# Kernel tuning notes

Measured on AMD Instinct MI355X. Metric: run time of the kernel, lower is better.

Reference implementation:

```python
import jax, jax.numpy as jnp
import numpy as np

N, E, F, HID, HEADS, L, OUT = 100000, 1600000, 16, 64, 2, 3, 200
EPS = 1e-5

def leaky(x, s):
    return jnp.where(x >= 0, x, s * x)

def layer_norm(x, g, b):
    m = jnp.mean(x, axis=-1, keepdims=True)
    v = jnp.mean(jnp.square(x - m), axis=-1, keepdims=True)
    return (x - m) * jax.lax.rsqrt(v + EPS) * g + b

def gat_conv(h, src, dst, W, a_src, a_dst, bias, n_nodes):
    # h: [N, HID]; W: [HID, HEADS*HID]; a_src/a_dst: [HEADS, HID]; bias: [HID]
    hp = (h @ W).reshape(n_nodes, HEADS, HID)            # [N, H, C]
    al_src = jnp.einsum('nhc,hc->nh', hp, a_src)          # [N, H]
    al_dst = jnp.einsum('nhc,hc->nh', hp, a_dst)
    e = leaky(al_src[src] + al_dst[dst], 0.2)             # [E', H]
    emax = jax.ops.segment_max(e, dst, num_segments=n_nodes)
    ee = jnp.exp(e - emax[dst])
    denom = jax.ops.segment_sum(ee, dst, num_segments=n_nodes)
    alpha = ee / (denom[dst] + 1e-16)                     # segment softmax over incoming edges
    msg = hp[src] * alpha[:, :, None]                     # [E', H, C]
    out = jax.ops.segment_sum(msg, dst, num_segments=n_nodes)  # [N, H, C]
    return jnp.mean(out, axis=1) + bias                   # concat=False -> head mean

def setup_inputs():
    key = jax.random.key(0)
    ks = jax.random.split(key, 16)
    rn = lambda k, s, sc=0.1: jax.random.normal(k, s, jnp.float32) * sc
    return {
        'x': jax.random.normal(ks[0], (N, F), jnp.float32),
        'edge_index': jax.random.randint(ks[1], (2, E), 0, N),
        'emb_w': rn(ks[2], (F, HID)), 'emb_b': jnp.zeros((HID,), jnp.float32),
        'emb_g': jnp.ones((HID,), jnp.float32), 'emb_beta': jnp.zeros((HID,), jnp.float32),
        'lin_w': rn(ks[3], (L, HID, HEADS * HID)),
        'att_src': rn(ks[4], (L, HEADS, HID)), 'att_dst': rn(ks[5], (L, HEADS, HID)),
        'conv_b': jnp.zeros((L, HID), jnp.float32),
        'ln_g': jnp.ones((L, HID), jnp.float32), 'ln_b': jnp.zeros((L, HID), jnp.float32),
        'fc1_w': rn(ks[6], (HID, HID)), 'fc1_b': jnp.zeros((HID,), jnp.float32),
        'fcn_g': jnp.ones((HID,), jnp.float32), 'fcn_b': jnp.zeros((HID,), jnp.float32),
        'fc2_w': rn(ks[7], (HID, OUT)), 'fc2_b': jnp.zeros((OUT,), jnp.float32),
    }

def reference(x, edge_index, emb_w, emb_b, emb_g, emb_beta, lin_w, att_src, att_dst,
              conv_b, ln_g, ln_b, fc1_w, fc1_b, fcn_g, fcn_b, fc2_w, fc2_b):
    n = x.shape[0]
    loops = jnp.arange(n)
    src = jnp.concatenate([edge_index[0], loops])  # PyG GATConv adds self-loops
    dst = jnp.concatenate([edge_index[1], loops])
    h = leaky(layer_norm(x @ emb_w + emb_b, emb_g, emb_beta), 0.1)
    for i in range(lin_w.shape[0]):
        h = gat_conv(h, src, dst, lin_w[i], att_src[i], att_dst[i], conv_b[i], n)
        h = leaky(layer_norm(h, ln_g[i], ln_b[i]), 0.1)
    g = jnp.mean(h, axis=0, keepdims=True)  # no batch vector -> global mean pool
    g = leaky(layer_norm(g @ fc1_w + fc1_b, fcn_g, fcn_b), 0.1)
    return jax.nn.sigmoid(g @ fc2_w + fc2_b)
```

## Files before the change

### kernel.cpp

```cpp
#include <hip/hip_runtime.h>
#include <hip/hip_bf16.h>
#include <math.h>

typedef __attribute__((ext_vector_type(8))) short short8v;
typedef __attribute__((ext_vector_type(4))) float float4v;

__device__ __forceinline__ float wsum(float v) {
#pragma unroll
  for (int s = 32; s > 0; s >>= 1) v += __shfl_xor(v, s, 64);
  return v;
}
__device__ __forceinline__ float bcast(float v, int l) {
  return __int_as_float(__builtin_amdgcn_readlane(__float_as_int(v), l));
}
__device__ __forceinline__ int bcasti(int v, int l) {
  return __builtin_amdgcn_readlane(v, l);
}
__device__ __forceinline__ unsigned bf16bits(float f) {
  unsigned u = __float_as_uint(f);
  return (u + 0x7fffu + ((u >> 16) & 1u)) >> 16;
}

__global__ void k_embed(const float* __restrict__ x, const float* __restrict__ w,
                        const float* __restrict__ b, const float* __restrict__ g,
                        const float* __restrict__ beta, short* __restrict__ hb, int n) {
  __shared__ float ws[16 * 64];
  for (int i = threadIdx.x; i < 16 * 64; i += blockDim.x) ws[i] = w[i];
  __syncthreads();
  int wid = (blockIdx.x * blockDim.x + threadIdx.x) >> 6;
  int lane = threadIdx.x & 63;
  if (wid >= n) return;
  const float* xr = x + (size_t)wid * 16;
  float acc = b[lane];
#pragma unroll
  for (int k = 0; k < 16; ++k) acc = fmaf(xr[k], ws[k * 64 + lane], acc);
  float mean = wsum(acc) * 0.015625f;
  float xc = acc - mean;
  float var = wsum(xc * xc) * 0.015625f;
  float y = xc * rsqrtf(var + 1e-5f) * g[lane] + beta[lane];
  y = (y >= 0.f) ? y : 0.1f * y;
  hb[(size_t)wid * 64 + lane] = (short)bf16bits(y);
}

__global__ void k_deg(const int* __restrict__ ei, int E, int n, int* __restrict__ deg,
                      int* __restrict__ pos) {
  int i = blockIdx.x * blockDim.x + threadIdx.x;
  int tot = E + n;
  if (i >= tot) return;
  int d = (i < E) ? ei[E + i] : (i - E);
  pos[i] = atomicAdd(&deg[d], 1);
}

__global__ void k_scanA(const int* __restrict__ deg, int n, int* __restrict__ texcl,
                        int* __restrict__ bsum) {
  __shared__ int sh[256];
  int bid = blockIdx.x, tid = threadIdx.x;
  int base = bid * 2048 + tid * 8;
  int s = 0;
#pragma unroll
  for (int i = 0; i < 8; ++i) {
    int idx = base + i;
    s += (idx < n) ? deg[idx] : 0;
  }
  sh[tid] = s;
  __syncthreads();
  for (int st = 1; st < 256; st <<= 1) {
    int t = (tid >= st) ? sh[tid - st] : 0;
    __syncthreads();
    sh[tid] += t;
    __syncthreads();
  }
  texcl[bid * 256 + tid] = sh[tid] - s;
  if (tid == 255) bsum[bid] = sh[255];
}

__global__ void k_scanB(int* __restrict__ bsum, int nb) {
  __shared__ int sh[256];
  int tid = threadIdx.x;
  int v = (tid < nb) ? bsum[tid] : 0;
  sh[tid] = v;
  __syncthreads();
  for (int st = 1; st < 256; st <<= 1) {
    int t = (tid >= st) ? sh[tid - st] : 0;
    __syncthreads();
    sh[tid] += t;
    __syncthreads();
  }
  if (tid < nb) bsum[tid] = sh[tid] - v;
}

__global__ void k_scanC(const int* __restrict__ deg, int n, const int* __restrict__ texcl,
                        const int* __restrict__ bsum, int* __restrict__ off, int total) {
  int bid = blockIdx.x, tid = threadIdx.x;
  int run = bsum[bid] + texcl[bid * 256 + tid];
  int base = bid * 2048 + tid * 8;
#pragma unroll
  for (int i = 0; i < 8; ++i) {
    int idx = base + i;
    if (idx < n) {
      off[idx] = run;
      run += deg[idx];
    }
  }
  if (bid == 0 && tid == 0) off[n] = total;
}

__global__ void k_scatter(const int* __restrict__ ei, int E, int n,
                          const int* __restrict__ off, const int* __restrict__ pos,
                          int* __restrict__ csr) {
  int i = blockIdx.x * blockDim.x + threadIdx.x;
  int tot = E + n;
  if (i >= tot) return;
  int s, d;
  if (i < E) { s = ei[i]; d = ei[E + i]; } else { s = i - E; d = i - E; }
  csr[off[d] + pos[i]] = s;
}

__global__ __launch_bounds__(256) void k_hp(
    const short* __restrict__ hb, const float* __restrict__ W,
    const float* __restrict__ asrc, const float* __restrict__ adst,
    unsigned* __restrict__ hp2, float2* __restrict__ al_s, float2* __restrict__ al_d,
    int n) {
  __shared__ short wlds[16 * 64 * 8];
  int tid = threadIdx.x;
  for (int idx = tid; idx < 1024; idx += 256) {
    int fr = idx >> 6;
    int ls = idx & 63;
    int kb = (fr >> 3) * 32 + (ls >> 4) * 8;
    int c = (fr & 7) * 16 + (ls & 15);
    short tmp[8];
#pragma unroll
    for (int j = 0; j < 8; ++j)
      tmp[j] = (short)bf16bits(W[(size_t)(kb + j) * 128 + c]);
    *reinterpret_cast<short8v*>(&wlds[idx * 8]) = *reinterpret_cast<const short8v*>(tmp);
  }
  __syncthreads();
  int lane = tid & 63;
  int nb = (blockIdx.x * 4 + (tid >> 6)) * 16;
  if (nb >= n) return;
  int col = lane & 15, kg = lane >> 4;
  int rowA = nb + col;
  if (rowA > n - 1) rowA = n - 1;
  const short8v* aptr = reinterpret_cast<const short8v*>(hb + (size_t)rowA * 64 + kg * 8);
  short8v af0 = aptr[0];
  short8v af1 = aptr[4];
  float ps0[4] = {0, 0, 0, 0}, ps1[4] = {0, 0, 0, 0};
  float pd0[4] = {0, 0, 0, 0}, pd1[4] = {0, 0, 0, 0};
#pragma unroll
  for (int ctp = 0; ctp < 4; ++ctp) {
    const short8v* bp0 = reinterpret_cast<const short8v*>(&wlds[((0 * 8 + ctp) * 64 + lane) * 8]);
    const short8v* bp1 = reinterpret_cast<const short8v*>(&wlds[((1 * 8 + ctp) * 64 + lane) * 8]);
    float4v accA = {0.f, 0.f, 0.f, 0.f};
    accA = __builtin_amdgcn_mfma_f32_16x16x32_bf16(af0, *bp0, accA, 0, 0, 0);
    accA = __builtin_amdgcn_mfma_f32_16x16x32_bf16(af1, *bp1, accA, 0, 0, 0);
    const short8v* bq0 = reinterpret_cast<const short8v*>(&wlds[((0 * 8 + ctp + 4) * 64 + lane) * 8]);
    const short8v* bq1 = reinterpret_cast<const short8v*>(&wlds[((1 * 8 + ctp + 4) * 64 + lane) * 8]);
    float4v accB = {0.f, 0.f, 0.f, 0.f};
    accB = __builtin_amdgcn_mfma_f32_16x16x32_bf16(af0, *bq0, accB, 0, 0, 0);
    accB = __builtin_amdgcn_mfma_f32_16x16x32_bf16(af1, *bq1, accB, 0, 0, 0);
    int c = ctp * 16 + col;
    float a_s0 = asrc[c], a_s1 = asrc[64 + c];
    float a_d0 = adst[c], a_d1 = adst[64 + c];
#pragma unroll
    for (int r = 0; r < 4; ++r) {
      int node = nb + kg * 4 + r;
      unsigned pk = bf16bits(accA[r]) | (bf16bits(accB[r]) << 16);
      if (node < n) hp2[(size_t)node * 64 + c] = pk;
      ps0[r] = fmaf(accA[r], a_s0, ps0[r]);
      ps1[r] = fmaf(accB[r], a_s1, ps1[r]);
      pd0[r] = fmaf(accA[r], a_d0, pd0[r]);
      pd1[r] = fmaf(accB[r], a_d1, pd1[r]);
    }
  }
#pragma unroll
  for (int m = 1; m < 16; m <<= 1) {
#pragma unroll
    for (int r = 0; r < 4; ++r) {
      ps0[r] += __shfl_xor(ps0[r], m, 64);
      ps1[r] += __shfl_xor(ps1[r], m, 64);
      pd0[r] += __shfl_xor(pd0[r], m, 64);
      pd1[r] += __shfl_xor(pd1[r], m, 64);
    }
  }
  if (col == 0) {
#pragma unroll
    for (int r = 0; r < 4; ++r) {
      int node = nb + kg * 4 + r;
      if (node < n) {
        al_s[node] = make_float2(ps0[r], ps1[r]);
        al_d[node] = make_float2(pd0[r], pd1[r]);
      }
    }
  }
}

__global__ void k_gat(const unsigned* __restrict__ hp2, const float* __restrict__ al_s,
                      const float* __restrict__ al_d, const int* __restrict__ off,
                      const int* __restrict__ csr, const float* __restrict__ bias,
                      const float* __restrict__ g, const float* __restrict__ b,
                      short* __restrict__ hb, int n) {
  int gw = (blockIdx.x * blockDim.x + threadIdx.x) >> 6;
  if (gw >= n) return;
  int node = __builtin_amdgcn_readfirstlane(gw);
  int lane = threadIdx.x & 63;
  const float2* al2 = (const float2*)al_s;
  float2 adv = ((const float2*)al_d)[node];
  int beg = off[node], end = off[node + 1];
  float acc0 = 0.f, acc1 = 0.f, dnl0 = 0.f, dnl1 = 0.f;
  for (int cb = beg; cb < end; cb += 64) {
    int jj = cb + lane;
    int sv = 0;
    float w0v = 0.f, w1v = 0.f;
    if (jj < end) {
      sv = csr[jj];
      float2 e = al2[sv];
      float e0 = e.x + adv.x; e0 = (e0 >= 0.f) ? e0 : 0.2f * e0;
      float e1 = e.y + adv.y; e1 = (e1 >= 0.f) ? e1 : 0.2f * e1;
      w0v = __expf(e0);
      w1v = __expf(e1);
    }
    dnl0 += w0v; dnl1 += w1v;
    int cnt = min(64, end - cb);
    int t = 0;
    for (; t + 4 <= cnt; t += 4) {
      int sA = bcasti(sv, t), sB = bcasti(sv, t + 1);
      int sC = bcasti(sv, t + 2), sD = bcasti(sv, t + 3);
      float wA0 = bcast(w0v, t), wA1 = bcast(w1v, t);
      float wB0 = bcast(w0v, t + 1), wB1 = bcast(w1v, t + 1);
      float wC0 = bcast(w0v, t + 2), wC1 = bcast(w1v, t + 2);
      float wD0 = bcast(w0v, t + 3), wD1 = bcast(w1v, t + 3);
      unsigned uA = hp2[(size_t)sA * 64 + lane];
      unsigned uB = hp2[(size_t)sB * 64 + lane];
      unsigned uC = hp2[(size_t)sC * 64 + lane];
      unsigned uD = hp2[(size_t)sD * 64 + lane];
      acc0 = fmaf(wA0, __uint_as_float(uA << 16), acc0);
      acc1 = fmaf(wA1, __uint_as_float(uA & 0xffff0000u), acc1);
      acc0 = fmaf(wB0, __uint_as_float(uB << 16), acc0);
      acc1 = fmaf(wB1, __uint_as_float(uB & 0xffff0000u), acc1);
      acc0 = fmaf(wC0, __uint_as_float(uC << 16), acc0);
      acc1 = fmaf(wC1, __uint_as_float(uC & 0xffff0000u), acc1);
      acc0 = fmaf(wD0, __uint_as_float(uD << 16), acc0);
      acc1 = fmaf(wD1, __uint_as_float(uD & 0xffff0000u), acc1);
    }
    for (; t < cnt; ++t) {
      int s = bcasti(sv, t);
      float w0 = bcast(w0v, t), w1 = bcast(w1v, t);
      unsigned u = hp2[(size_t)s * 64 + lane];
      acc0 = fmaf(w0, __uint_as_float(u << 16), acc0);
      acc1 = fmaf(w1, __uint_as_float(u & 0xffff0000u), acc1);
    }
  }
  float dn0 = wsum(dnl0), dn1 = wsum(dnl1);
  float oc = 0.5f * (acc0 / (dn0 + 1e-16f) + acc1 / (dn1 + 1e-16f)) + bias[lane];
  float mean = wsum(oc) * 0.015625f;
  float xc = oc - mean;
  float var = wsum(xc * xc) * 0.015625f;
  float y = xc * rsqrtf(var + 1e-5f) * g[lane] + b[lane];
  y = (y >= 0.f) ? y : 0.1f * y;
  hb[(size_t)node * 64 + lane] = (short)bf16bits(y);
}

__global__ void k_pool(const short* __restrict__ hb, float* __restrict__ gsum, int n) {
  __shared__ float sh[256];
  int col = threadIdx.x & 63;
  int rw = threadIdx.x >> 6;
  float acc = 0.f;
  for (long r = (long)blockIdx.x * 4 + rw; r < n; r += (long)gridDim.x * 4) {
    unsigned u = (unsigned)(unsigned short)hb[r * 64 + col];
    acc += __uint_as_float(u << 16);
  }
  sh[threadIdx.x] = acc;
  __syncthreads();
  if (threadIdx.x < 64) {
    float s = sh[threadIdx.x] + sh[64 + threadIdx.x] + sh[128 + threadIdx.x] +
              sh[192 + threadIdx.x];
    atomicAdd(&gsum[col], s);
  }
}

__global__ void k_head(const float* __restrict__ gsum, const float* __restrict__ fc1w,
                       const float* __restrict__ fc1b, const float* __restrict__ fng,
                       const float* __restrict__ fnb, const float* __restrict__ fc2w,
                       const float* __restrict__ fc2b, float* __restrict__ out,
                       float invN) {
  __shared__ float t[64];
  __shared__ float gl[64];
  int tid = threadIdx.x;
  if (tid < 64) gl[tid] = gsum[tid] * invN;
  __syncthreads();
  if (tid < 64) {
    float z = fc1b[tid];
    for (int k = 0; k < 64; ++k) z = fmaf(gl[k], fc1w[k * 64 + tid], z);
    float mean = wsum(z) * 0.015625f;
    float xc = z - mean;
    float var = wsum(xc * xc) * 0.015625f;
    float y = xc * rsqrtf(var + 1e-5f) * fng[tid] + fnb[tid];
    t[tid] = (y >= 0.f) ? y : 0.1f * y;
  }
  __syncthreads();
  if (tid < 200) {
    float o = fc2b[tid];
    for (int k = 0; k < 64; ++k) o = fmaf(t[k], fc2w[k * 200 + tid], o);
    out[tid] = 1.f / (1.f + expf(-o));
  }
}

extern "C" void kernel_launch(void* const* d_in, const int* in_sizes, int n_in,
                              void* d_out, int out_size, void* d_ws, size_t ws_size,
                              hipStream_t stream) {
  const float* x      = (const float*)d_in[0];
  const int*   ei     = (const int*)d_in[1];
  const float* emb_w  = (const float*)d_in[2];
  const float* emb_b  = (const float*)d_in[3];
  const float* emb_g  = (const float*)d_in[4];
  const float* emb_be = (const float*)d_in[5];
  const float* lin_w  = (const float*)d_in[6];
  const float* att_s  = (const float*)d_in[7];
  const float* att_d  = (const float*)d_in[8];
  const float* conv_b = (const float*)d_in[9];
  const float* ln_g   = (const float*)d_in[10];
  const float* ln_b   = (const float*)d_in[11];
  const float* fc1_w  = (const float*)d_in[12];
  const float* fc1_b  = (const float*)d_in[13];
  const float* fcn_g  = (const float*)d_in[14];
  const float* fcn_b  = (const float*)d_in[15];
  const float* fc2_w  = (const float*)d_in[16];
  const float* fc2_b  = (const float*)d_in[17];
  float* out = (float*)d_out;

  int N = in_sizes[0] / 16;
  int E = in_sizes[1] / 2;
  int tot = E + N;
  int nb_scan = (N + 2047) / 2048;

  char* p = (char*)d_ws;
  auto alloc = [&](size_t bytes) {
    char* r = p;
    p += (bytes + 255) & ~(size_t)255;
    return r;
  };
  short*    hb    = (short*)alloc((size_t)N * 64 * 2);
  unsigned* hp2   = (unsigned*)alloc((size_t)N * 64 * 4);
  float2*   al_s  = (float2*)alloc((size_t)N * 8);
  float2*   al_d  = (float2*)alloc((size_t)N * 8);
  int*      deg   = (int*)alloc((size_t)N * 4);
  int*      off   = (int*)alloc((size_t)(N + 1) * 4);
  int*      pos   = (int*)alloc((size_t)tot * 4);
  int*      csr   = (int*)alloc((size_t)tot * 4);
  float*    gsum  = (float*)alloc(64 * 4);
  int*      texcl = (int*)alloc((size_t)nb_scan * 256 * 4);
  int*      bsum  = (int*)alloc((size_t)nb_scan * 4);

  hipMemsetAsync(deg, 0, (size_t)N * 4, stream);
  hipMemsetAsync(gsum, 0, 64 * 4, stream);

  int eb = (tot + 255) / 256;
  k_deg<<<eb, 256, 0, stream>>>(ei, E, N, deg, pos);
  k_scanA<<<nb_scan, 256, 0, stream>>>(deg, N, texcl, bsum);
  k_scanB<<<1, 256, 0, stream>>>(bsum, nb_scan);
  k_scanC<<<nb_scan, 256, 0, stream>>>(deg, N, texcl, bsum, off, tot);
  k_scatter<<<eb, 256, 0, stream>>>(ei, E, N, off, pos, csr);

  int nbe = (N + 3) / 4;
  k_embed<<<nbe, 256, 0, stream>>>(x, emb_w, emb_b, emb_g, emb_be, hb, N);

  int nbh = (N + 63) / 64;
  for (int l = 0; l < 3; ++l) {
    k_hp<<<nbh, 256, 0, stream>>>(hb, lin_w + (size_t)l * 64 * 128, att_s + l * 128,
                                  att_d + l * 128, hp2, al_s, al_d, N);
    k_gat<<<nbe, 256, 0, stream>>>(hp2, (const float*)al_s, (const float*)al_d, off,
                                   csr, conv_b + l * 64, ln_g + l * 64, ln_b + l * 64,
                                   hb, N);
  }

  k_pool<<<1024, 256, 0, stream>>>(hb, gsum, N);
  k_head<<<1, 256, 0, stream>>>(gsum, fc1_w, fc1_b, fcn_g, fcn_b, fc2_w, fc2_b, out,
                                1.0f / (float)N);
}
```

Measured before the change: 519.6 us.

## Stage edge records in LDS and gather two edges per wave step

Each wave now writes its chunk of edge records (source index and the two head weights) to shared memory instead of broadcasting them with readlane. Each half-wave then handles a different edge per step, with every lane loading 8 bytes (two bf16 pairs) of the source row. The two halves' partial sums are combined at the end with cross-lane shuffles. This aims to cut scalar broadcast overhead and halve the number of gather load instructions per edge. In exchange it adds LDS traffic, a small shuffle epilogue, and relies on wave-local ordering of the LDS buffer with no explicit barrier.

Measured after the change: 524.9 us. No clear change (+1.0%).

```diff
diff --git a/kernel.cpp b/kernel.cpp
--- a/kernel.cpp
+++ b/kernel.cpp
@@ -9,12 +9,6 @@
 #pragma unroll
   for (int s = 32; s > 0; s >>= 1) v += __shfl_xor(v, s, 64);
   return v;
-}
-__device__ __forceinline__ float bcast(float v, int l) {
-  return __int_as_float(__builtin_amdgcn_readlane(__float_as_int(v), l));
-}
-__device__ __forceinline__ int bcasti(int v, int l) {
-  return __builtin_amdgcn_readlane(v, l);
 }
 __device__ __forceinline__ unsigned bf16bits(float f) {
   unsigned u = __float_as_uint(f);
@@ -199,14 +193,19 @@
                       const int* __restrict__ csr, const float* __restrict__ bias,
                       const float* __restrict__ g, const float* __restrict__ b,
                       short* __restrict__ hb, int n) {
+  __shared__ uint4 recs[4][64];
   int gw = (blockIdx.x * blockDim.x + threadIdx.x) >> 6;
   if (gw >= n) return;
   int node = __builtin_amdgcn_readfirstlane(gw);
   int lane = threadIdx.x & 63;
+  int wslot = (threadIdx.x >> 6) & 3;
+  int hl = lane & 31;
+  int halfSel = lane >> 5;
   const float2* al2 = (const float2*)al_s;
   float2 adv = ((const float2*)al_d)[node];
   int beg = off[node], end = off[node + 1];
-  float acc0 = 0.f, acc1 = 0.f, dnl0 = 0.f, dnl1 = 0.f;
+  float a00 = 0.f, a01 = 0.f, a10 = 0.f, a11 = 0.f;
+  float dnl0 = 0.f, dnl1 = 0.f;
   for (int cb = beg; cb < end; cb += 64) {
     int jj = cb + lane;
     int sv = 0;
@@ -220,36 +219,46 @@
       w1v = __expf(e1);
     }
     dnl0 += w0v; dnl1 += w1v;
+    recs[wslot][lane] =
+        make_uint4((unsigned)sv, __float_as_uint(w0v), __float_as_uint(w1v), 0u);
+    const uint4* rb = &recs[wslot][0];
     int cnt = min(64, end - cb);
     int t = 0;
     for (; t + 4 <= cnt; t += 4) {
-      int sA = bcasti(sv, t), sB = bcasti(sv, t + 1);
-      int sC = bcasti(sv, t + 2), sD = bcasti(sv, t + 3);
-      float wA0 = bcast(w0v, t), wA1 = bcast(w1v, t);
-      float wB0 = bcast(w0v, t + 1), wB1 = bcast(w1v, t + 1);
-      float wC0 = bcast(w0v, t + 2), wC1 = bcast(w1v, t + 2);
-      float wD0 = bcast(w0v, t + 3), wD1 = bcast(w1v, t + 3);
-      unsigned uA = hp2[(size_t)sA * 64 + lane];
-      unsigned uB = hp2[(size_t)sB * 64 + lane];
-      unsigned uC = hp2[(size_t)sC * 64 + lane];
-      unsigned uD = hp2[(size_t)sD * 64 + lane];
-      acc0 = fmaf(wA0, __uint_as_float(uA << 16), acc0);
-      acc1 = fmaf(wA1, __uint_as_float(uA & 0xffff0000u), acc1);
-      acc0 = fmaf(wB0, __uint_as_float(uB << 16), acc0);
-      acc1 = fmaf(wB1, __uint_as_float(uB & 0xffff0000u), acc1);
-      acc0 = fmaf(wC0, __uint_as_float(uC << 16), acc0);
-      acc1 = fmaf(wC1, __uint_as_float(uC & 0xffff0000u), acc1);
-      acc0 = fmaf(wD0, __uint_as_float(uD << 16), acc0);
-      acc1 = fmaf(wD1, __uint_as_float(uD & 0xffff0000u), acc1);
-    }
-    for (; t < cnt; ++t) {
-      int s = bcasti(sv, t);
-      float w0 = bcast(w0v, t), w1 = bcast(w1v, t);
-      unsigned u = hp2[(size_t)s * 64 + lane];
-      acc0 = fmaf(w0, __uint_as_float(u << 16), acc0);
-      acc1 = fmaf(w1, __uint_as_float(u & 0xffff0000u), acc1);
-    }
-  }
+      uint4 rA = rb[t + halfSel];
+      uint4 rB = rb[t + 2 + halfSel];
+      uint2 uA = *reinterpret_cast<const uint2*>(hp2 + (size_t)rA.x * 64 + 2 * hl);
+      uint2 uB = *reinterpret_cast<const uint2*>(hp2 + (size_t)rB.x * 64 + 2 * hl);
+      float wA0 = __uint_as_float(rA.y), wA1 = __uint_as_float(rA.z);
+      float wB0 = __uint_as_float(rB.y), wB1 = __uint_as_float(rB.z);
+      a00 = fmaf(wA0, __uint_as_float(uA.x << 16), a00);
+      a01 = fmaf(wA1, __uint_as_float(uA.x & 0xffff0000u), a01);
+      a10 = fmaf(wA0, __uint_as_float(uA.y << 16), a10);
+      a11 = fmaf(wA1, __uint_as_float(uA.y & 0xffff0000u), a11);
+      a00 = fmaf(wB0, __uint_as_float(uB.x << 16), a00);
+      a01 = fmaf(wB1, __uint_as_float(uB.x & 0xffff0000u), a01);
+      a10 = fmaf(wB0, __uint_as_float(uB.y << 16), a10);
+      a11 = fmaf(wB1, __uint_as_float(uB.y & 0xffff0000u), a11);
+    }
+    for (; t < cnt; t += 2) {
+      uint4 r = rb[t + halfSel];
+      uint2 u = *reinterpret_cast<const uint2*>(hp2 + (size_t)r.x * 64 + 2 * hl);
+      float w0 = __uint_as_float(r.y), w1 = __uint_as_float(r.z);
+      a00 = fmaf(w0, __uint_as_float(u.x << 16), a00);
+      a01 = fmaf(w1, __uint_as_float(u.x & 0xffff0000u), a01);
+      a10 = fmaf(w0, __uint_as_float(u.y << 16), a10);
+      a11 = fmaf(w1, __uint_as_float(u.y & 0xffff0000u), a11);
+    }
+  }
+  a00 += __shfl_xor(a00, 32, 64);
+  a01 += __shfl_xor(a01, 32, 64);
+  a10 += __shfl_xor(a10, 32, 64);
+  a11 += __shfl_xor(a11, 32, 64);
+  int src = lane >> 1;
+  float e0h0 = __shfl(a00, src, 64), e1h0 = __shfl(a10, src, 64);
+  float e0h1 = __shfl(a01, src, 64), e1h1 = __shfl(a11, src, 64);
+  float acc0 = (lane & 1) ? e1h0 : e0h0;
+  float acc1 = (lane & 1) ? e1h1 : e0h1;
   float dn0 = wsum(dnl0), dn1 = wsum(dnl1);
   float oc = 0.5f * (acc0 / (dn0 + 1e-16f) + acc1 / (dn1 + 1e-16f)) + bias[lane];
   float mean = wsum(oc) * 0.015625f;
```
